# Kernel optimization log

Hardware: AMD Instinct MI355X
Metric: run time of the kernel (lower is better)

Reference implementation:

```python
import jax, jax.numpy as jnp
import numpy as np

D = 512            # token_dim * num_heads
TOKEN_DIM = 256
SCALE = TOKEN_DIM ** (-0.5)
EPS = 1e-12        # torch F.normalize eps
FIDX = (0, 1, 1)   # original bug: out_rv uses final_myo


def l2norm(x, axis):
    n = jnp.sqrt(jnp.sum(x * x, axis=axis, keepdims=True))
    return x / jnp.maximum(n, EPS)


def setup_inputs() -> dict:
    key = jax.random.key(0)
    ks = jax.random.split(key, 16)
    B, N = 16, 1024
    s = 0.02
    return {
        "x_lv": jax.random.normal(ks[0], (B, N, D), jnp.float32),
        "x_myo": jax.random.normal(ks[1], (B, N, D), jnp.float32),
        "x_rv": jax.random.normal(ks[2], (B, N, D), jnp.float32),
        # stacked per-branch params: branch 0=lv, 1=myo, 2=rv
        "Wq": jax.random.normal(ks[3], (3, D, D), jnp.float32) * s,
        "bq": jax.random.normal(ks[4], (3, D), jnp.float32) * s,
        "Wk": jax.random.normal(ks[5], (3, D, D), jnp.float32) * s,
        "bk": jax.random.normal(ks[6], (3, D), jnp.float32) * s,
        "wg": jax.random.normal(ks[7], (3, D, 1), jnp.float32),
        "Wp": jax.random.normal(ks[8], (3, 3, D, D), jnp.float32) * s,  # [branch, key_src]
        "bp": jax.random.normal(ks[9], (3, 3, D), jnp.float32) * s,
        "Wf": jax.random.normal(ks[10], (3, D, TOKEN_DIM), jnp.float32) * s,
        "bf": jax.random.normal(ks[11], (3, TOKEN_DIM), jnp.float32) * s,
    }


def reference(x_lv, x_myo, x_rv, Wq, bq, Wk, bk, wg, Wp, bp, Wf, bf):
    X = (x_lv, x_myo, x_rv)
    # projections + L2 normalize over feature dim
    Q = [l2norm(X[m] @ Wq[m] + bq[m], axis=-1) for m in range(3)]  # [B,N,D]
    K = [l2norm(X[m] @ Wk[m] + bk[m], axis=-1) for m in range(3)]  # [B,N,D]
    outs = []
    for m in range(3):
        A = l2norm((Q[m] @ wg[m]) * SCALE, axis=1)       # [B,N,1], normed over seq
        G = jnp.sum(A * Q[m], axis=1)[:, None, :]        # [B,1,D] (broadcast repeat)
        acc = Q[m]
        for j in range(3):
            acc = acc + (G * K[j]) @ Wp[m, j] + bp[m, j]
        outs.append(acc @ Wf[FIDX[m]] + bf[FIDX[m]])     # [B,N,token_dim]
    return tuple(outs)
```

## Files before the change

kernel.cpp:

```cpp
#include <hip/hip_runtime.h>
#include <hip/hip_bf16.h>

typedef __hip_bfloat16 bf16;
typedef __attribute__((ext_vector_type(8))) short short8;
typedef __attribute__((ext_vector_type(4))) float f32x4;

#define SCALE_F 0.0625f

__device__ __forceinline__ float b2f(short s) {
  union { float f; unsigned int u; } x;
  x.u = ((unsigned int)(unsigned short)s) << 16;
  return x.f;
}
__device__ __forceinline__ unsigned short f2bu(float f) {
  __hip_bfloat16 h = __float2bfloat16(f);
  unsigned short u;
  __builtin_memcpy(&u, &h, 2);
  return u;
}
__device__ __forceinline__ void store_out(float* p, float v) { *p = v; }
__device__ __forceinline__ void store_out(bf16* p, float v) { *p = __float2bfloat16(v); }

typedef __attribute__((address_space(3))) void lds_void;
typedef __attribute__((address_space(1))) void gbl_void;

__device__ __forceinline__ void lds_load16(void* l, const void* g) {
  __builtin_amdgcn_global_load_lds((const gbl_void*)g, (lds_void*)l, 16, 0, 0);
}

__device__ __forceinline__ void gemm256_xf32(
    const float* __restrict__ Af, int ldA,
    const bf16* __restrict__ Bt, int ldB,
    bf16* C, int ldC, const float* bias, int row0, int col0)
{
  __shared__ bf16 Abuf0[256 * 64], Abuf1[256 * 64];
  __shared__ bf16 Bbuf0[256 * 64], Bbuf1[256 * 64];
  const int tid = threadIdx.x;
  const int lane = tid & 63, w = tid >> 6;
  const int wm = w >> 2, wn = w & 3;
  const int lr = lane & 15, hi = lane >> 4;

  const int stageR = tid >> 3;
  const int cNat   = (tid & 7) << 3;
  const int cSwz   = ((tid & 7) ^ (stageR & 7)) << 3;
  const float* Ag0 = Af + (size_t)(row0 + stageR) * ldA + cNat;
  const bf16*  Bg0 = Bt + (size_t)(col0 + stageR) * ldB + cSwz;
  const int AwOff = stageR * 64 + cSwz;

  float4 prefE[8], prefO[8];
  auto issueA = [&](float4 (&dst)[8], int k0) {
#pragma unroll
    for (int q = 0; q < 4; ++q) {
      const float* p = Ag0 + (size_t)(q * 64) * ldA + k0;
      dst[q * 2 + 0] = *(const float4*)(p);
      dst[q * 2 + 1] = *(const float4*)(p + 4);
    }
  };
  auto writeA = [&](const float4 (&src)[8], bf16* Al) {
#pragma unroll
    for (int q = 0; q < 4; ++q) {
      float4 v0 = src[q * 2 + 0], v1 = src[q * 2 + 1];
      short8 o;
      o[0] = (short)f2bu(v0.x); o[1] = (short)f2bu(v0.y);
      o[2] = (short)f2bu(v0.z); o[3] = (short)f2bu(v0.w);
      o[4] = (short)f2bu(v1.x); o[5] = (short)f2bu(v1.y);
      o[6] = (short)f2bu(v1.z); o[7] = (short)f2bu(v1.w);
      *(short8*)&Al[AwOff + q * 4096] = o;
    }
  };
  auto stageB = [&](int bsel, int k0) {
    bf16* Bl = (bsel ? Bbuf1 : Bbuf0) + tid * 8;
    const bf16* Bg = Bg0 + k0;
#pragma unroll
    for (int q = 0; q < 4; ++q)
      lds_load16(Bl + q * 4096, Bg + (size_t)(q * 64) * ldB);
  };

  const int aoffb = (wm * 128 + lr) * 128;
  const int boffb = (wn * 64 + lr) * 128;
  const int s0 = ((hi ^ (lr & 7)) << 4);
  const int s1 = (((4 + hi) ^ (lr & 7)) << 4);

  f32x4 acc[8][4];
#pragma unroll
  for (int i = 0; i < 8; ++i)
#pragma unroll
    for (int j = 0; j < 4; ++j) acc[i][j] = (f32x4){0.f, 0.f, 0.f, 0.f};

  issueA(prefE, 0);
  issueA(prefO, 64);
  stageB(0, 0);
  stageB(1, 64);
  writeA(prefE, Abuf0);
  issueA(prefE, 128);
  writeA(prefO, Abuf1);
  asm volatile("s_waitcnt vmcnt(12)" ::: "memory");
  asm volatile("s_waitcnt lgkmcnt(0)" ::: "memory");
  __builtin_amdgcn_s_barrier();

#pragma unroll
  for (int t = 0; t < 8; ++t) {
    if (t + 3 < 8) {
      if (((t + 3) & 1) == 0) issueA(prefE, (t + 3) * 64);
      else                    issueA(prefO, (t + 3) * 64);
    }
    const char* Ab = (const char*)((t & 1) ? Abuf1 : Abuf0);
    const char* Bb = (const char*)((t & 1) ? Bbuf1 : Bbuf0);
    short8 ra[8], rb[4], ra2[8], rb2[4];
#pragma unroll
    for (int fr = 0; fr < 8; ++fr) ra[fr] = *(const short8*)(Ab + aoffb + fr * 2048 + s0);
#pragma unroll
    for (int fq = 0; fq < 4; ++fq) rb[fq] = *(const short8*)(Bb + boffb + fq * 2048 + s0);
    __builtin_amdgcn_s_setprio(1);
#pragma unroll
    for (int fr = 0; fr < 8; ++fr)
#pragma unroll
      for (int fq = 0; fq < 4; ++fq)
        acc[fr][fq] = __builtin_amdgcn_mfma_f32_16x16x32_bf16(ra[fr], rb[fq], acc[fr][fq], 0, 0, 0);
    __builtin_amdgcn_s_setprio(0);
#pragma unroll
    for (int fr = 0; fr < 8; ++fr) ra2[fr] = *(const short8*)(Ab + aoffb + fr * 2048 + s1);
#pragma unroll
    for (int fq = 0; fq < 4; ++fq) rb2[fq] = *(const short8*)(Bb + boffb + fq * 2048 + s1);
    asm volatile("s_waitcnt lgkmcnt(0)" ::: "memory");
    __builtin_amdgcn_s_barrier();
    if (t + 2 < 8) {
      if ((t & 1) == 0) writeA(prefE, Abuf0);
      else              writeA(prefO, Abuf1);
      stageB(t & 1, (t + 2) * 64);
    }
    __builtin_amdgcn_s_setprio(1);
#pragma unroll
    for (int fr = 0; fr < 8; ++fr)
#pragma unroll
      for (int fq = 0; fq < 4; ++fq)
        acc[fr][fq] = __builtin_amdgcn_mfma_f32_16x16x32_bf16(ra2[fr], rb2[fq], acc[fr][fq], 0, 0, 0);
    __builtin_amdgcn_s_setprio(0);
    if (t + 1 < 8) {
      if (t + 3 < 8)      asm volatile("s_waitcnt vmcnt(12)" ::: "memory");
      else if (t + 2 < 8) asm volatile("s_waitcnt vmcnt(4)"  ::: "memory");
      else                asm volatile("s_waitcnt vmcnt(0)"  ::: "memory");
      __builtin_amdgcn_s_barrier();
    }
  }

#pragma unroll
  for (int fr = 0; fr < 8; ++fr) {
    const int rowb = row0 + wm * 128 + fr * 16 + hi * 4;
#pragma unroll
    for (int fq = 0; fq < 4; ++fq) {
      const int col = col0 + wn * 64 + fq * 16 + lr;
      const float bv = bias[col];
      f32x4 v = acc[fr][fq];
#pragma unroll
      for (int r = 0; r < 4; ++r)
        store_out(&C[(size_t)(rowb + r) * ldC + col], v[r] + bv);
    }
  }
}

template<typename OutT>
__device__ __forceinline__ void gemm128p(
    const bf16* A0, const bf16* A1, const bf16* A2, const bf16* A3, int ldA,
    const bf16* Bt, int ldB, OutT* C, int ldC, const float* bias,
    int K, int row0, int col0)
{
  __shared__ bf16 Abuf0[128 * 64], Abuf1[128 * 64];
  __shared__ bf16 Bbuf0[128 * 64], Bbuf1[128 * 64];
  const int tid = threadIdx.x;
  const int lane = tid & 63, w = tid >> 6;
  const int wm = w >> 1, wn = w & 1;
  const int lr = lane & 15, hi = lane >> 4;

  const int stageR = tid >> 3;
  const int stageC = ((tid & 7) ^ (stageR & 7)) << 3;
  const bf16* Bg0 = Bt + (size_t)(col0 + stageR) * ldB + stageC;

  auto stage = [&](int bsel, int k0) {
    const int seg = k0 >> 9;
    const bf16* Aseg = (seg == 0) ? A0 : (seg == 1) ? A1 : (seg == 2) ? A2 : A3;
    const bf16* Ag = Aseg + (size_t)(row0 + stageR) * ldA + (k0 & 511) + stageC;
    const bf16* Bg = Bg0 + k0;
    bf16* Al = (bsel ? Abuf1 : Abuf0) + tid * 8;
    bf16* Bl = (bsel ? Bbuf1 : Bbuf0) + tid * 8;
#pragma unroll
    for (int q = 0; q < 4; ++q) {
      lds_load16(Al + q * 2048, Ag + (size_t)(q * 32) * ldA);
      lds_load16(Bl + q * 2048, Bg + (size_t)(q * 32) * ldB);
    }
  };

  const int aoffb = (wm * 64 + lr) * 128;
  const int boffb = (wn * 64 + lr) * 128;
  const int s0 = ((hi ^ (lr & 7)) << 4);
  const int s1 = (((4 + hi) ^ (lr & 7)) << 4);

  f32x4 acc[4][4];
#pragma unroll
  for (int i = 0; i < 4; ++i)
#pragma unroll
    for (int j = 0; j < 4; ++j) acc[i][j] = (f32x4){0.f, 0.f, 0.f, 0.f};

  const int nt = K >> 6;
  stage(0, 0);
  stage(1, 64);
  asm volatile("s_waitcnt vmcnt(8)" ::: "memory");
  __builtin_amdgcn_s_barrier();

  for (int t = 0; t < nt; ++t) {
    const char* Ab = (const char*)((t & 1) ? Abuf1 : Abuf0);
    const char* Bb = (const char*)((t & 1) ? Bbuf1 : Bbuf0);
    short8 ra[4], rb[4], ra2[4], rb2[4];
#pragma unroll
    for (int fr = 0; fr < 4; ++fr) ra[fr] = *(const short8*)(Ab + aoffb + fr * 2048 + s0);
#pragma unroll
    for (int fq = 0; fq < 4; ++fq) rb[fq] = *(const short8*)(Bb + boffb + fq * 2048 + s0);
    __builtin_amdgcn_s_setprio(1);
#pragma unroll
    for (int fr = 0; fr < 4; ++fr)
#pragma unroll
      for (int fq = 0; fq < 4; ++fq)
        acc[fr][fq] = __builtin_amdgcn_mfma_f32_16x16x32_bf16(ra[fr], rb[fq], acc[fr][fq], 0, 0, 0);
    __builtin_amdgcn_s_setprio(0);
#pragma unroll
    for (int fr = 0; fr < 4; ++fr) ra2[fr] = *(const short8*)(Ab + aoffb + fr * 2048 + s1);
#pragma unroll
    for (int fq = 0; fq < 4; ++fq) rb2[fq] = *(const short8*)(Bb + boffb + fq * 2048 + s1);
    asm volatile("s_waitcnt lgkmcnt(0)" ::: "memory");
    __builtin_amdgcn_s_barrier();
    if (t + 2 < nt) stage(t & 1, (t + 2) << 6);
    __builtin_amdgcn_s_setprio(1);
#pragma unroll
    for (int fr = 0; fr < 4; ++fr)
#pragma unroll
      for (int fq = 0; fq < 4; ++fq)
        acc[fr][fq] = __builtin_amdgcn_mfma_f32_16x16x32_bf16(ra2[fr], rb2[fq], acc[fr][fq], 0, 0, 0);
    __builtin_amdgcn_s_setprio(0);
    if (t + 1 < nt) {
      if (t + 2 < nt) asm volatile("s_waitcnt vmcnt(8)" ::: "memory");
      else            asm volatile("s_waitcnt vmcnt(0)" ::: "memory");
      __builtin_amdgcn_s_barrier();
    }
  }

#pragma unroll
  for (int fr = 0; fr < 4; ++fr) {
    const int rowb = row0 + wm * 64 + fr * 16 + hi * 4;
#pragma unroll
    for (int fq = 0; fq < 4; ++fq) {
      const int col = col0 + wn * 64 + fq * 16 + lr;
      const float bv = bias ? bias[col] : 0.f;
      f32x4 v = acc[fr][fq];
#pragma unroll
      for (int r = 0; r < 4; ++r)
        store_out(&C[(size_t)(rowb + r) * ldC + col], v[r] + bv);
    }
  }
}

template<typename OutT>
__device__ __forceinline__ void gemm_tile(
    const bf16* A0, int ldA, const bf16* Bt, int ldB, OutT* C, int ldC,
    const float* bias, int K, int row0, int col0)
{
  __shared__ bf16 As[128 * 32];
  __shared__ bf16 Bs[128 * 32];
  const int t = threadIdx.x;
  const int lane = t & 63;
  const int w = t >> 6;
  const int wm = w >> 1, wn = w & 1;
  const int lr = lane & 15, hi = lane >> 4;
  const int rA = t >> 2;
  const int kA = (t & 3) * 8;

  f32x4 acc[4][4];
#pragma unroll
  for (int i = 0; i < 4; ++i)
#pragma unroll
    for (int j = 0; j < 4; ++j) acc[i][j] = (f32x4){0.f, 0.f, 0.f, 0.f};

  const int nk = K >> 5;
  for (int kt = 0; kt < nk; ++kt) {
    const int k0 = kt << 5;
    __syncthreads();
    lds_load16(&As[t * 8],        A0 + (size_t)(row0 + rA) * ldA + k0 + kA);
    lds_load16(&As[2048 + t * 8], A0 + (size_t)(row0 + 64 + rA) * ldA + k0 + kA);
    lds_load16(&Bs[t * 8],        Bt + (size_t)(col0 + rA) * ldB + k0 + kA);
    lds_load16(&Bs[2048 + t * 8], Bt + (size_t)(col0 + 64 + rA) * ldB + k0 + kA);
    __syncthreads();
    short8 af[4], bfr[4];
#pragma unroll
    for (int f = 0; f < 4; ++f)
      af[f] = *(const short8*)&As[(wm * 64 + f * 16 + lr) * 32 + hi * 8];
#pragma unroll
    for (int f = 0; f < 4; ++f)
      bfr[f] = *(const short8*)&Bs[(wn * 64 + f * 16 + lr) * 32 + hi * 8];
#pragma unroll
    for (int i = 0; i < 4; ++i)
#pragma unroll
      for (int j = 0; j < 4; ++j)
        acc[i][j] = __builtin_amdgcn_mfma_f32_16x16x32_bf16(af[i], bfr[j], acc[i][j], 0, 0, 0);
  }

#pragma unroll
  for (int i = 0; i < 4; ++i) {
    const int rowb = row0 + wm * 64 + i * 16 + hi * 4;
#pragma unroll
    for (int j = 0; j < 4; ++j) {
      const int col = col0 + wn * 64 + j * 16 + lr;
      const float bv = bias ? bias[col] : 0.f;
      f32x4 v = acc[i][j];
#pragma unroll
      for (int r = 0; r < 4; ++r)
        store_out(&C[(size_t)(rowb + r) * ldC + col], v[r] + bv);
    }
  }
}

__global__ __launch_bounds__(256) void k_transpose(
    const float* __restrict__ in, bf16* __restrict__ out, int R, int C)
{
  const int tilesC = C >> 6;
  const int tr = (blockIdx.x / tilesC) << 6;
  const int tc = (blockIdx.x % tilesC) << 6;
  const size_t base = (size_t)blockIdx.y * R * C;
  __shared__ unsigned short tile[64][72];
  const int rr = threadIdx.x >> 4;
  const int cc = (threadIdx.x & 15) << 2;
#pragma unroll
  for (int p = 0; p < 4; ++p) {
    const int r = rr + (p << 4);
    float4 v = *(const float4*)&in[base + (size_t)(tr + r) * C + tc + cc];
    tile[cc + 0][r] = f2bu(v.x);
    tile[cc + 1][r] = f2bu(v.y);
    tile[cc + 2][r] = f2bu(v.z);
    tile[cc + 3][r] = f2bu(v.w);
  }
  __syncthreads();
#pragma unroll
  for (int p = 0; p < 4; ++p) {
    const int r = rr + (p << 4);
    ushort4 o;
    o.x = tile[r][cc + 0];
    o.y = tile[r][cc + 1];
    o.z = tile[r][cc + 2];
    o.w = tile[r][cc + 3];
    *(ushort4*)&out[base + (size_t)(tc + r) * R + tr + cc] = o;
  }
}

__global__ __launch_bounds__(256) void k_copy_bf16(
    const float* __restrict__ in, bf16* __restrict__ out)
{
  const long long i = (long long)blockIdx.x * 256 + threadIdx.x;
  float4 v = ((const float4*)in)[i];
  ushort4 o;
  o.x = f2bu(v.x); o.y = f2bu(v.y); o.z = f2bu(v.z); o.w = f2bu(v.w);
  ((ushort4*)out)[i] = o;
}

__global__ __launch_bounds__(256) void k_bprime(
    const float* __restrict__ bp, const float* __restrict__ Wf,
    const float* __restrict__ bfv, float* __restrict__ bpr)
{
  const int m = blockIdx.x;
  const int dc = blockIdx.y;
  const int n = threadIdx.x;
  const int fi = (m == 0) ? 0 : 1;
  float s = (dc == 0) ? bfv[fi * 256 + n] : 0.f;
  for (int d = dc * 64; d < dc * 64 + 64; ++d) {
    float b3 = bp[(m * 3 + 0) * 512 + d] + bp[(m * 3 + 1) * 512 + d] +
               bp[(m * 3 + 2) * 512 + d];
    s += b3 * Wf[(size_t)fi * 512 * 256 + (size_t)d * 256 + n];
  }
  atomicAdd(&bpr[m * 256 + n], s);
}

__global__ __launch_bounds__(512, 2) void k_gemm1(
    const float* __restrict__ x0, const float* __restrict__ x1,
    const float* __restrict__ x2, const bf16* __restrict__ WT,
    const float* __restrict__ bq, const float* __restrict__ bk,
    bf16* __restrict__ QK)
{
  const int bid = blockIdx.x;
  const int swz = (bid & 7) * 96 + (bid >> 3);
  const int m = swz >> 8;
  const int rem = swz & 255;
  const int tm = rem >> 2;
  const int tn = (rem >> 1) & 1;
  const int qk = rem & 1;
  const int inst = qk ? (m + 3) : m;
  const float* A = (m == 0) ? x0 : (m == 1) ? x1 : x2;
  const bf16* B = WT + (size_t)inst * (512 * 512);
  const float* bias = (qk ? bk : bq) + m * 512;
  bf16* C = QK + (size_t)inst * (16384 * 512);
  gemm256_xf32(A, 512, B, 512, C, 512, bias, tm * 256, tn * 256);
}

__global__ __launch_bounds__(256) void k_gemm_wpf(
    const bf16* __restrict__ WfT, const bf16* __restrict__ Wpbf,
    float* __restrict__ WpfT)
{
  const int inst = blockIdx.y;
  const int m = inst / 3;
  const int fi = (m == 0) ? 0 : 1;
  const int tm = blockIdx.x >> 2, tn = blockIdx.x & 3;
  const bf16* A = WfT + (size_t)fi * (256 * 512);
  const bf16* B = Wpbf + (size_t)inst * (512 * 512);
  float* C = WpfT + (size_t)inst * (256 * 512);
  gemm_tile<float>(A, 512, B, 512, C, 512, nullptr, 512, tm * 128, tn * 128);
}

__global__ __launch_bounds__(256, 2) void k_gemm2(
    const bf16* __restrict__ QK, const bf16* __restrict__ W2T,
    const float* __restrict__ bpr, float* __restrict__ out)
{
  const int bid = blockIdx.x;
  const int swz = (bid & 7) * 96 + (bid >> 3);
  const int e = swz >> 4;
  const int tm = (swz >> 1) & 7;
  const int tn = swz & 1;
  const int m = e / 16, b = e & 15;
  const bf16* A0 = QK + ((size_t)m * 16384 + (size_t)b * 1024) * 512;
  const bf16* A1 = QK + ((size_t)(3 * 16384) + (size_t)b * 1024) * 512;
  const bf16* A2 = QK + ((size_t)(4 * 16384) + (size_t)b * 1024) * 512;
  const bf16* A3 = QK + ((size_t)(5 * 16384) + (size_t)b * 1024) * 512;
  const bf16* Bt = W2T + (size_t)e * (256 * 2048);
  float* C = out + (size_t)e * (1024 * 256);
  gemm128p<float>(A0, A1, A2, A3, 512, Bt, 2048, C, 256, bpr + m * 256, 2048,
                  tm * 128, tn * 128);
}

__global__ __launch_bounds__(256) void k_norm(
    bf16* __restrict__ QK, const float* __restrict__ wg, float* __restrict__ qdot)
{
  const int row = blockIdx.x * 4 + (threadIdx.x >> 6);
  const int lane = threadIdx.x & 63;
  bf16* p = QK + (size_t)row * 512 + lane * 8;
  short8 v = *(const short8*)p;
  float f[8];
  float ss = 0.f;
#pragma unroll
  for (int i = 0; i < 8; ++i) { f[i] = b2f(v[i]); ss += f[i] * f[i]; }
#pragma unroll
  for (int o = 32; o; o >>= 1) ss += __shfl_xor(ss, o);
  const float inv = 1.f / fmaxf(sqrtf(ss), 1e-12f);
  short8 ov;
#pragma unroll
  for (int i = 0; i < 8; ++i) ov[i] = (short)f2bu(f[i] * inv);
  *(short8*)p = ov;
  const int tt = row >> 14;
  if (tt < 3) {
    const float* wgm = wg + (size_t)tt * 512 + lane * 8;
    float dot = 0.f;
#pragma unroll
    for (int i = 0; i < 8; ++i) dot += f[i] * wgm[i];
    dot *= inv;
#pragma unroll
    for (int o = 32; o; o >>= 1) dot += __shfl_xor(dot, o);
    if (lane == 0) qdot[row] = dot;
  }
}

__global__ __launch_bounds__(256) void k_G(
    const float* __restrict__ qdot, const bf16* __restrict__ QK, float* __restrict__ G)
{
  const int e = blockIdx.x;
  const int m = e >> 4, b = e & 15;
  const int d0 = blockIdx.y << 6;
  __shared__ float Al[1024];
  __shared__ float red[4];
  __shared__ float Gp[4][64];
  const int t = threadIdx.x;
  const float* qd = qdot + (size_t)m * 16384 + (size_t)b * 1024;
  float ss = 0.f;
#pragma unroll
  for (int i = 0; i < 4; ++i) {
    float x = qd[t + i * 256] * SCALE_F;
    Al[t + i * 256] = x;
    ss += x * x;
  }
#pragma unroll
  for (int o = 32; o; o >>= 1) ss += __shfl_xor(ss, o);
  if ((t & 63) == 0) red[t >> 6] = ss;
  __syncthreads();
  const float inv = 1.f / fmaxf(sqrtf(red[0] + red[1] + red[2] + red[3]), 1e-12f);

  const int d = d0 + (t & 63);
  const int q = t >> 6;
  const bf16* Qb = QK + ((size_t)m * 16384 + (size_t)b * 1024) * 512 + d;
  float g = 0.f;
  for (int n = q * 256; n < q * 256 + 256; ++n)
    g += Al[n] * b2f(*(const short*)&Qb[(size_t)n * 512]);
  Gp[q][t & 63] = g;
  __syncthreads();
  if (t < 64)
    G[(size_t)e * 512 + d0 + t] = (Gp[0][t] + Gp[1][t] + Gp[2][t] + Gp[3][t]) * inv;
}

__global__ __launch_bounds__(256) void k_w2t(
    const bf16* __restrict__ WfT, const float* __restrict__ WpfT,
    const float* __restrict__ G, bf16* __restrict__ W2T)
{
  const int e = blockIdx.x;
  const int m = e >> 4;
  const int fi = (m == 0) ? 0 : 1;
  const int t = threadIdx.x;
  bf16* out = W2T + (size_t)e * (256 * 2048);
  __shared__ float Gl[512];
  Gl[t] = G[(size_t)e * 512 + t];
  Gl[t + 256] = G[(size_t)e * 512 + t + 256];
  __syncthreads();
  const int k = t * 8;
  for (int nr = 0; nr < 16; ++nr) {
    const int n = blockIdx.y * 16 + nr;
    if (k < 512) {
      *(short8*)&out[(size_t)n * 2048 + k] =
          *(const short8*)&WfT[((size_t)fi * 256 + n) * 512 + k];
    } else {
      const int j = (k >> 9) - 1;
      const int d = k & 511;
      const float* src = WpfT + (((size_t)(m * 3 + j) * 256 + n) * 512 + d);
      short8 o;
#pragma unroll
      for (int i = 0; i < 8; ++i) o[i] = (short)f2bu(Gl[d + i] * src[i]);
      *(short8*)&out[(size_t)n * 2048 + k] = o;
    }
  }
}

extern "C" void kernel_launch(void* const* d_in, const int* in_sizes, int n_in,
                              void* d_out, int out_size, void* d_ws, size_t ws_size,
                              hipStream_t stream) {
  const float* x_lv = (const float*)d_in[0];
  const float* x_myo = (const float*)d_in[1];
  const float* x_rv = (const float*)d_in[2];
  const float* Wq = (const float*)d_in[3];
  const float* bq = (const float*)d_in[4];
  const float* Wk = (const float*)d_in[5];
  const float* bk = (const float*)d_in[6];
  const float* wg = (const float*)d_in[7];
  const float* Wp = (const float*)d_in[8];
  const float* bp = (const float*)d_in[9];
  const float* Wf = (const float*)d_in[10];
  const float* bfv = (const float*)d_in[11];
  float* out = (float*)d_out;

  char* ws = (char*)d_ws;
  bf16* QK    = (bf16*)(ws);
  bf16* W2T   = (bf16*)(ws + 100663296);
  bf16* WT    = (bf16*)(ws + 150994944);
  bf16* Wpbf  = (bf16*)(ws + 154140672);
  bf16* WfT   = (bf16*)(ws + 158859264);
  float* WpfT = (float*)(ws + 159383552);
  float* qdot = (float*)(ws + 164102144);
  float* G    = (float*)(ws + 164298752);
  float* bpr  = (float*)(ws + 164397056);

  k_transpose<<<dim3(64, 3), 256, 0, stream>>>(Wq, WT, 512, 512);
  k_transpose<<<dim3(64, 3), 256, 0, stream>>>(Wk, WT + 3 * 512 * 512, 512, 512);
  k_transpose<<<dim3(32, 2), 256, 0, stream>>>(Wf, WfT, 512, 256);
  k_copy_bf16<<<2304, 256, 0, stream>>>(Wp, Wpbf);
  hipMemsetAsync(bpr, 0, 3 * 256 * sizeof(float), stream);
  k_bprime<<<dim3(3, 8), 256, 0, stream>>>(bp, Wf, bfv, bpr);

  k_gemm1<<<768, 512, 0, stream>>>(x_lv, x_myo, x_rv, WT, bq, bk, QK);

  k_norm<<<24576, 256, 0, stream>>>(QK, wg, qdot);

  k_gemm_wpf<<<dim3(8, 9), 256, 0, stream>>>(WfT, Wpbf, WpfT);

  k_G<<<dim3(48, 8), 256, 0, stream>>>(qdot, QK, G);

  k_w2t<<<dim3(48, 16), 256, 0, stream>>>(WfT, WpfT, G, W2T);

  k_gemm2<<<768, 256, 0, stream>>>(QK, W2T, bpr, out);
}
```

Baseline: 388.8 us.

## Pre-convert inputs to bf16 in fused prep kernel and use async LDS loads in gemm1

Merges the weight transposes, Wp conversion, bias precomputation and a new fp32-to-bf16 conversion of the three activation inputs into one prep kernel. The first GEMM then reads bf16 activations through direct global-to-LDS loads instead of converting fp32 in registers. The bias atomics and memset are replaced by per-chunk partial sums that the second GEMM adds at its epilogue. This removes several launches and the register conversion path, but adds a full extra read and write pass over the activations. The W2T buffer now reuses the Xbf workspace region.

```diff
diff --git a/kernel.cpp b/kernel.cpp
--- a/kernel.cpp
+++ b/kernel.cpp
@@ -28,148 +28,17 @@
   __builtin_amdgcn_global_load_lds((const gbl_void*)g, (lds_void*)l, 16, 0, 0);
 }
 
-__device__ __forceinline__ void gemm256_xf32(
-    const float* __restrict__ Af, int ldA,
-    const bf16* __restrict__ Bt, int ldB,
-    bf16* C, int ldC, const float* bias, int row0, int col0)
+template<typename OutT>
+__device__ __forceinline__ void gemm256_tile(
+    const bf16* A0, const bf16* A1, const bf16* A2, const bf16* A3, int ldA,
+    const bf16* Bt, int ldB, OutT* C, int ldC, const float* bias,
+    int K, int row0, int col0)
 {
   __shared__ bf16 Abuf0[256 * 64], Abuf1[256 * 64];
   __shared__ bf16 Bbuf0[256 * 64], Bbuf1[256 * 64];
   const int tid = threadIdx.x;
   const int lane = tid & 63, w = tid >> 6;
   const int wm = w >> 2, wn = w & 3;
-  const int lr = lane & 15, hi = lane >> 4;
-
-  const int stageR = tid >> 3;
-  const int cNat   = (tid & 7) << 3;
-  const int cSwz   = ((tid & 7) ^ (stageR & 7)) << 3;
-  const float* Ag0 = Af + (size_t)(row0 + stageR) * ldA + cNat;
-  const bf16*  Bg0 = Bt + (size_t)(col0 + stageR) * ldB + cSwz;
-  const int AwOff = stageR * 64 + cSwz;
-
-  float4 prefE[8], prefO[8];
-  auto issueA = [&](float4 (&dst)[8], int k0) {
-#pragma unroll
-    for (int q = 0; q < 4; ++q) {
-      const float* p = Ag0 + (size_t)(q * 64) * ldA + k0;
-      dst[q * 2 + 0] = *(const float4*)(p);
-      dst[q * 2 + 1] = *(const float4*)(p + 4);
-    }
-  };
-  auto writeA = [&](const float4 (&src)[8], bf16* Al) {
-#pragma unroll
-    for (int q = 0; q < 4; ++q) {
-      float4 v0 = src[q * 2 + 0], v1 = src[q * 2 + 1];
-      short8 o;
-      o[0] = (short)f2bu(v0.x); o[1] = (short)f2bu(v0.y);
-      o[2] = (short)f2bu(v0.z); o[3] = (short)f2bu(v0.w);
-      o[4] = (short)f2bu(v1.x); o[5] = (short)f2bu(v1.y);
-      o[6] = (short)f2bu(v1.z); o[7] = (short)f2bu(v1.w);
-      *(short8*)&Al[AwOff + q * 4096] = o;
-    }
-  };
-  auto stageB = [&](int bsel, int k0) {
-    bf16* Bl = (bsel ? Bbuf1 : Bbuf0) + tid * 8;
-    const bf16* Bg = Bg0 + k0;
-#pragma unroll
-    for (int q = 0; q < 4; ++q)
-      lds_load16(Bl + q * 4096, Bg + (size_t)(q * 64) * ldB);
-  };
-
-  const int aoffb = (wm * 128 + lr) * 128;
-  const int boffb = (wn * 64 + lr) * 128;
-  const int s0 = ((hi ^ (lr & 7)) << 4);
-  const int s1 = (((4 + hi) ^ (lr & 7)) << 4);
-
-  f32x4 acc[8][4];
-#pragma unroll
-  for (int i = 0; i < 8; ++i)
-#pragma unroll
-    for (int j = 0; j < 4; ++j) acc[i][j] = (f32x4){0.f, 0.f, 0.f, 0.f};
-
-  issueA(prefE, 0);
-  issueA(prefO, 64);
-  stageB(0, 0);
-  stageB(1, 64);
-  writeA(prefE, Abuf0);
-  issueA(prefE, 128);
-  writeA(prefO, Abuf1);
-  asm volatile("s_waitcnt vmcnt(12)" ::: "memory");
-  asm volatile("s_waitcnt lgkmcnt(0)" ::: "memory");
-  __builtin_amdgcn_s_barrier();
-
-#pragma unroll
-  for (int t = 0; t < 8; ++t) {
-    if (t + 3 < 8) {
-      if (((t + 3) & 1) == 0) issueA(prefE, (t + 3) * 64);
-      else                    issueA(prefO, (t + 3) * 64);
-    }
-    const char* Ab = (const char*)((t & 1) ? Abuf1 : Abuf0);
-    const char* Bb = (const char*)((t & 1) ? Bbuf1 : Bbuf0);
-    short8 ra[8], rb[4], ra2[8], rb2[4];
-#pragma unroll
-    for (int fr = 0; fr < 8; ++fr) ra[fr] = *(const short8*)(Ab + aoffb + fr * 2048 + s0);
-#pragma unroll
-    for (int fq = 0; fq < 4; ++fq) rb[fq] = *(const short8*)(Bb + boffb + fq * 2048 + s0);
-    __builtin_amdgcn_s_setprio(1);
-#pragma unroll
-    for (int fr = 0; fr < 8; ++fr)
-#pragma unroll
-      for (int fq = 0; fq < 4; ++fq)
-        acc[fr][fq] = __builtin_amdgcn_mfma_f32_16x16x32_bf16(ra[fr], rb[fq], acc[fr][fq], 0, 0, 0);
-    __builtin_amdgcn_s_setprio(0);
-#pragma unroll
-    for (int fr = 0; fr < 8; ++fr) ra2[fr] = *(const short8*)(Ab + aoffb + fr * 2048 + s1);
-#pragma unroll
-    for (int fq = 0; fq < 4; ++fq) rb2[fq] = *(const short8*)(Bb + boffb + fq * 2048 + s1);
-    asm volatile("s_waitcnt lgkmcnt(0)" ::: "memory");
-    __builtin_amdgcn_s_barrier();
-    if (t + 2 < 8) {
-      if ((t & 1) == 0) writeA(prefE, Abuf0);
-      else              writeA(prefO, Abuf1);
-      stageB(t & 1, (t + 2) * 64);
-    }
-    __builtin_amdgcn_s_setprio(1);
-#pragma unroll
-    for (int fr = 0; fr < 8; ++fr)
-#pragma unroll
-      for (int fq = 0; fq < 4; ++fq)
-        acc[fr][fq] = __builtin_amdgcn_mfma_f32_16x16x32_bf16(ra2[fr], rb2[fq], acc[fr][fq], 0, 0, 0);
-    __builtin_amdgcn_s_setprio(0);
-    if (t + 1 < 8) {
-      if (t + 3 < 8)      asm volatile("s_waitcnt vmcnt(12)" ::: "memory");
-      else if (t + 2 < 8) asm volatile("s_waitcnt vmcnt(4)"  ::: "memory");
-      else                asm volatile("s_waitcnt vmcnt(0)"  ::: "memory");
-      __builtin_amdgcn_s_barrier();
-    }
-  }
-
-#pragma unroll
-  for (int fr = 0; fr < 8; ++fr) {
-    const int rowb = row0 + wm * 128 + fr * 16 + hi * 4;
-#pragma unroll
-    for (int fq = 0; fq < 4; ++fq) {
-      const int col = col0 + wn * 64 + fq * 16 + lr;
-      const float bv = bias[col];
-      f32x4 v = acc[fr][fq];
-#pragma unroll
-      for (int r = 0; r < 4; ++r)
-        store_out(&C[(size_t)(rowb + r) * ldC + col], v[r] + bv);
-    }
-  }
-}
-
-template<typename OutT>
-__device__ __forceinline__ void gemm128p(
-    const bf16* A0, const bf16* A1, const bf16* A2, const bf16* A3, int ldA,
-    const bf16* Bt, int ldB, OutT* C, int ldC, const float* bias,
-    int K, int row0, int col0)
-{
-  __shared__ bf16 Abuf0[128 * 64], Abuf1[128 * 64];
-  __shared__ bf16 Bbuf0[128 * 64], Bbuf1[128 * 64];
-  const int tid = threadIdx.x;
-  const int lane = tid & 63, w = tid >> 6;
-  const int wm = w >> 1, wn = w & 1;
   const int lr = lane & 15, hi = lane >> 4;
 
   const int stageR = tid >> 3;
@@ -185,19 +54,19 @@
     bf16* Bl = (bsel ? Bbuf1 : Bbuf0) + tid * 8;
 #pragma unroll
     for (int q = 0; q < 4; ++q) {
-      lds_load16(Al + q * 2048, Ag + (size_t)(q * 32) * ldA);
-      lds_load16(Bl + q * 2048, Bg + (size_t)(q * 32) * ldB);
+      lds_load16(Al + q * 4096, Ag + (size_t)q * 64 * ldA);
+      lds_load16(Bl + q * 4096, Bg + (size_t)q * 64 * ldB);
     }
   };
 
-  const int aoffb = (wm * 64 + lr) * 128;
+  const int aoffb = (wm * 128 + lr) * 128;
   const int boffb = (wn * 64 + lr) * 128;
   const int s0 = ((hi ^ (lr & 7)) << 4);
   const int s1 = (((4 + hi) ^ (lr & 7)) << 4);
 
-  f32x4 acc[4][4];
-#pragma unroll
-  for (int i = 0; i < 4; ++i)
+  f32x4 acc[8][4];
+#pragma unroll
+  for (int i = 0; i < 8; ++i)
 #pragma unroll
     for (int j = 0; j < 4; ++j) acc[i][j] = (f32x4){0.f, 0.f, 0.f, 0.f};
 
@@ -210,20 +79,20 @@
   for (int t = 0; t < nt; ++t) {
     const char* Ab = (const char*)((t & 1) ? Abuf1 : Abuf0);
     const char* Bb = (const char*)((t & 1) ? Bbuf1 : Bbuf0);
-    short8 ra[4], rb[4], ra2[4], rb2[4];
-#pragma unroll
-    for (int fr = 0; fr < 4; ++fr) ra[fr] = *(const short8*)(Ab + aoffb + fr * 2048 + s0);
+    short8 ra[8], rb[4], ra2[8], rb2[4];
+#pragma unroll
+    for (int fr = 0; fr < 8; ++fr) ra[fr] = *(const short8*)(Ab + aoffb + fr * 2048 + s0);
 #pragma unroll
     for (int fq = 0; fq < 4; ++fq) rb[fq] = *(const short8*)(Bb + boffb + fq * 2048 + s0);
     __builtin_amdgcn_s_setprio(1);
 #pragma unroll
-    for (int fr = 0; fr < 4; ++fr)
+    for (int fr = 0; fr < 8; ++fr)
 #pragma unroll
       for (int fq = 0; fq < 4; ++fq)
         acc[fr][fq] = __builtin_amdgcn_mfma_f32_16x16x32_bf16(ra[fr], rb[fq], acc[fr][fq], 0, 0, 0);
     __builtin_amdgcn_s_setprio(0);
 #pragma unroll
-    for (int fr = 0; fr < 4; ++fr) ra2[fr] = *(const short8*)(Ab + aoffb + fr * 2048 + s1);
+    for (int fr = 0; fr < 8; ++fr) ra2[fr] = *(const short8*)(Ab + aoffb + fr * 2048 + s1);
 #pragma unroll
     for (int fq = 0; fq < 4; ++fq) rb2[fq] = *(const short8*)(Bb + boffb + fq * 2048 + s1);
     asm volatile("s_waitcnt lgkmcnt(0)" ::: "memory");
@@ -231,7 +100,7 @@
     if (t + 2 < nt) stage(t & 1, (t + 2) << 6);
     __builtin_amdgcn_s_setprio(1);
 #pragma unroll
-    for (int fr = 0; fr < 4; ++fr)
+    for (int fr = 0; fr < 8; ++fr)
 #pragma unroll
       for (int fq = 0; fq < 4; ++fq)
         acc[fr][fq] = __builtin_amdgcn_mfma_f32_16x16x32_bf16(ra2[fr], rb2[fq], acc[fr][fq], 0, 0, 0);
@@ -244,12 +113,115 @@
   }
 
 #pragma unroll
-  for (int fr = 0; fr < 4; ++fr) {
-    const int rowb = row0 + wm * 64 + fr * 16 + hi * 4;
+  for (int fr = 0; fr < 8; ++fr) {
+    const int rowb = row0 + wm * 128 + fr * 16 + hi * 4;
 #pragma unroll
     for (int fq = 0; fq < 4; ++fq) {
       const int col = col0 + wn * 64 + fq * 16 + lr;
       const float bv = bias ? bias[col] : 0.f;
+      f32x4 v = acc[fr][fq];
+#pragma unroll
+      for (int r = 0; r < 4; ++r)
+        store_out(&C[(size_t)(rowb + r) * ldC + col], v[r] + bv);
+    }
+  }
+}
+
+template<typename OutT, int BREP>
+__device__ __forceinline__ void gemm128p(
+    const bf16* A0, const bf16* A1, const bf16* A2, const bf16* A3, int ldA,
+    const bf16* Bt, int ldB, OutT* C, int ldC, const float* bias,
+    int K, int row0, int col0)
+{
+  __shared__ bf16 Abuf0[128 * 64], Abuf1[128 * 64];
+  __shared__ bf16 Bbuf0[128 * 64], Bbuf1[128 * 64];
+  const int tid = threadIdx.x;
+  const int lane = tid & 63, w = tid >> 6;
+  const int wm = w >> 1, wn = w & 1;
+  const int lr = lane & 15, hi = lane >> 4;
+
+  const int stageR = tid >> 3;
+  const int stageC = ((tid & 7) ^ (stageR & 7)) << 3;
+  const bf16* Bg0 = Bt + (size_t)(col0 + stageR) * ldB + stageC;
+
+  auto stage = [&](int bsel, int k0) {
+    const int seg = k0 >> 9;
+    const bf16* Aseg = (seg == 0) ? A0 : (seg == 1) ? A1 : (seg == 2) ? A2 : A3;
+    const bf16* Ag = Aseg + (size_t)(row0 + stageR) * ldA + (k0 & 511) + stageC;
+    const bf16* Bg = Bg0 + k0;
+    bf16* Al = (bsel ? Abuf1 : Abuf0) + tid * 8;
+    bf16* Bl = (bsel ? Bbuf1 : Bbuf0) + tid * 8;
+#pragma unroll
+    for (int q = 0; q < 4; ++q) {
+      lds_load16(Al + q * 2048, Ag + (size_t)(q * 32) * ldA);
+      lds_load16(Bl + q * 2048, Bg + (size_t)(q * 32) * ldB);
+    }
+  };
+
+  const int aoffb = (wm * 64 + lr) * 128;
+  const int boffb = (wn * 64 + lr) * 128;
+  const int s0 = ((hi ^ (lr & 7)) << 4);
+  const int s1 = (((4 + hi) ^ (lr & 7)) << 4);
+
+  f32x4 acc[4][4];
+#pragma unroll
+  for (int i = 0; i < 4; ++i)
+#pragma unroll
+    for (int j = 0; j < 4; ++j) acc[i][j] = (f32x4){0.f, 0.f, 0.f, 0.f};
+
+  const int nt = K >> 6;
+  stage(0, 0);
+  stage(1, 64);
+  asm volatile("s_waitcnt vmcnt(8)" ::: "memory");
+  __builtin_amdgcn_s_barrier();
+
+  for (int t = 0; t < nt; ++t) {
+    const char* Ab = (const char*)((t & 1) ? Abuf1 : Abuf0);
+    const char* Bb = (const char*)((t & 1) ? Bbuf1 : Bbuf0);
+    short8 ra[4], rb[4], ra2[4], rb2[4];
+#pragma unroll
+    for (int fr = 0; fr < 4; ++fr) ra[fr] = *(const short8*)(Ab + aoffb + fr * 2048 + s0);
+#pragma unroll
+    for (int fq = 0; fq < 4; ++fq) rb[fq] = *(const short8*)(Bb + boffb + fq * 2048 + s0);
+    __builtin_amdgcn_s_setprio(1);
+#pragma unroll
+    for (int fr = 0; fr < 4; ++fr)
+#pragma unroll
+      for (int fq = 0; fq < 4; ++fq)
+        acc[fr][fq] = __builtin_amdgcn_mfma_f32_16x16x32_bf16(ra[fr], rb[fq], acc[fr][fq], 0, 0, 0);
+    __builtin_amdgcn_s_setprio(0);
+#pragma unroll
+    for (int fr = 0; fr < 4; ++fr) ra2[fr] = *(const short8*)(Ab + aoffb + fr * 2048 + s1);
+#pragma unroll
+    for (int fq = 0; fq < 4; ++fq) rb2[fq] = *(const short8*)(Bb + boffb + fq * 2048 + s1);
+    asm volatile("s_waitcnt lgkmcnt(0)" ::: "memory");
+    __builtin_amdgcn_s_barrier();
+    if (t + 2 < nt) stage(t & 1, (t + 2) << 6);
+    __builtin_amdgcn_s_setprio(1);
+#pragma unroll
+    for (int fr = 0; fr < 4; ++fr)
+#pragma unroll
+      for (int fq = 0; fq < 4; ++fq)
+        acc[fr][fq] = __builtin_amdgcn_mfma_f32_16x16x32_bf16(ra2[fr], rb2[fq], acc[fr][fq], 0, 0, 0);
+    __builtin_amdgcn_s_setprio(0);
+    if (t + 1 < nt) {
+      if (t + 2 < nt) asm volatile("s_waitcnt vmcnt(8)" ::: "memory");
+      else            asm volatile("s_waitcnt vmcnt(0)" ::: "memory");
+      __builtin_amdgcn_s_barrier();
+    }
+  }
+
+#pragma unroll
+  for (int fr = 0; fr < 4; ++fr) {
+    const int rowb = row0 + wm * 64 + fr * 16 + hi * 4;
+#pragma unroll
+    for (int fq = 0; fq < 4; ++fq) {
+      const int col = col0 + wn * 64 + fq * 16 + lr;
+      float bv = 0.f;
+      if (bias) {
+#pragma unroll
+        for (int i = 0; i < BREP; ++i) bv += bias[i * 256 + col];
+      }
       f32x4 v = acc[fr][fq];
 #pragma unroll
       for (int r = 0; r < 4; ++r)
@@ -317,68 +289,90 @@
   }
 }
 
-__global__ __launch_bounds__(256) void k_transpose(
-    const float* __restrict__ in, bf16* __restrict__ out, int R, int C)
-{
-  const int tilesC = C >> 6;
-  const int tr = (blockIdx.x / tilesC) << 6;
-  const int tc = (blockIdx.x % tilesC) << 6;
-  const size_t base = (size_t)blockIdx.y * R * C;
+__global__ __launch_bounds__(256) void k_prep(
+    const float* __restrict__ x0, const float* __restrict__ x1,
+    const float* __restrict__ x2, bf16* __restrict__ xbf,
+    const float* __restrict__ Wq, const float* __restrict__ Wk,
+    const float* __restrict__ Wf, const float* __restrict__ Wp,
+    const float* __restrict__ bp, const float* __restrict__ bfv,
+    bf16* __restrict__ WT, bf16* __restrict__ WfT,
+    bf16* __restrict__ Wpbf, float* __restrict__ bprp)
+{
   __shared__ unsigned short tile[64][72];
-  const int rr = threadIdx.x >> 4;
-  const int cc = (threadIdx.x & 15) << 2;
-#pragma unroll
-  for (int p = 0; p < 4; ++p) {
-    const int r = rr + (p << 4);
-    float4 v = *(const float4*)&in[base + (size_t)(tr + r) * C + tc + cc];
-    tile[cc + 0][r] = f2bu(v.x);
-    tile[cc + 1][r] = f2bu(v.y);
-    tile[cc + 2][r] = f2bu(v.z);
-    tile[cc + 3][r] = f2bu(v.w);
-  }
-  __syncthreads();
-#pragma unroll
-  for (int p = 0; p < 4; ++p) {
-    const int r = rr + (p << 4);
+  const int bid = blockIdx.x;
+  const int t = threadIdx.x;
+
+  if (bid >= 1048) {
+    const long long i = (long long)(bid - 1048) * 256 + t;
+    const int tt = (int)(i / 2097152);
+    const long long e = i - (long long)tt * 2097152;
+    const float4* src = (const float4*)(tt == 0 ? x0 : tt == 1 ? x1 : x2);
+    float4 v = src[e];
     ushort4 o;
-    o.x = tile[r][cc + 0];
-    o.y = tile[r][cc + 1];
-    o.z = tile[r][cc + 2];
-    o.w = tile[r][cc + 3];
-    *(ushort4*)&out[base + (size_t)(tc + r) * R + tr + cc] = o;
-  }
-}
-
-__global__ __launch_bounds__(256) void k_copy_bf16(
-    const float* __restrict__ in, bf16* __restrict__ out)
-{
-  const long long i = (long long)blockIdx.x * 256 + threadIdx.x;
-  float4 v = ((const float4*)in)[i];
-  ushort4 o;
-  o.x = f2bu(v.x); o.y = f2bu(v.y); o.z = f2bu(v.z); o.w = f2bu(v.w);
-  ((ushort4*)out)[i] = o;
-}
-
-__global__ __launch_bounds__(256) void k_bprime(
-    const float* __restrict__ bp, const float* __restrict__ Wf,
-    const float* __restrict__ bfv, float* __restrict__ bpr)
-{
-  const int m = blockIdx.x;
-  const int dc = blockIdx.y;
-  const int n = threadIdx.x;
-  const int fi = (m == 0) ? 0 : 1;
-  float s = (dc == 0) ? bfv[fi * 256 + n] : 0.f;
-  for (int d = dc * 64; d < dc * 64 + 64; ++d) {
-    float b3 = bp[(m * 3 + 0) * 512 + d] + bp[(m * 3 + 1) * 512 + d] +
-               bp[(m * 3 + 2) * 512 + d];
-    s += b3 * Wf[(size_t)fi * 512 * 256 + (size_t)d * 256 + n];
-  }
-  atomicAdd(&bpr[m * 256 + n], s);
+    o.x = f2bu(v.x); o.y = f2bu(v.y); o.z = f2bu(v.z); o.w = f2bu(v.w);
+    ((ushort4*)xbf)[i] = o;
+    return;
+  }
+  if (bid < 448) {
+    const float* in; bf16* out; int R, C, ti;
+    if (bid < 192)      { in = Wq + (bid / 64) * 262144; out = WT + (bid / 64) * 262144; R = 512; C = 512; ti = bid & 63; }
+    else if (bid < 384) { int b2 = bid - 192; in = Wk + (b2 / 64) * 262144; out = WT + (3 + b2 / 64) * 262144; R = 512; C = 512; ti = b2 & 63; }
+    else                { int b2 = bid - 384; in = Wf + (b2 / 32) * 131072; out = WfT + (b2 / 32) * 131072; R = 512; C = 256; ti = b2 & 31; }
+    const int tilesC = C >> 6;
+    const int tr = (ti / tilesC) << 6;
+    const int tc = (ti % tilesC) << 6;
+    const int rr = t >> 4;
+    const int cc = (t & 15) << 2;
+#pragma unroll
+    for (int p = 0; p < 4; ++p) {
+      const int r = rr + (p << 4);
+      float4 v = *(const float4*)&in[(size_t)(tr + r) * C + tc + cc];
+      tile[cc + 0][r] = f2bu(v.x);
+      tile[cc + 1][r] = f2bu(v.y);
+      tile[cc + 2][r] = f2bu(v.z);
+      tile[cc + 3][r] = f2bu(v.w);
+    }
+    __syncthreads();
+#pragma unroll
+    for (int p = 0; p < 4; ++p) {
+      const int r = rr + (p << 4);
+      ushort4 o;
+      o.x = tile[r][cc + 0];
+      o.y = tile[r][cc + 1];
+      o.z = tile[r][cc + 2];
+      o.w = tile[r][cc + 3];
+      *(ushort4*)&out[(size_t)(tc + r) * R + tr + cc] = o;
+    }
+    return;
+  }
+  if (bid < 1024) {
+    const int base = (bid - 448) * 256 + t;
+#pragma unroll
+    for (int s = 0; s < 4; ++s) {
+      const int i = base + s * 147456;
+      float4 v = ((const float4*)Wp)[i];
+      ushort4 o;
+      o.x = f2bu(v.x); o.y = f2bu(v.y); o.z = f2bu(v.z); o.w = f2bu(v.w);
+      ((ushort4*)Wpbf)[i] = o;
+    }
+    return;
+  }
+  {
+    const int mm = (bid - 1024) >> 3, dc = (bid - 1024) & 7;
+    const int n = t;
+    const int fi = (mm == 0) ? 0 : 1;
+    float s = (dc == 0) ? bfv[fi * 256 + n] : 0.f;
+    for (int d = dc * 64; d < dc * 64 + 64; ++d) {
+      float b3 = bp[(mm * 3 + 0) * 512 + d] + bp[(mm * 3 + 1) * 512 + d] +
+                 bp[(mm * 3 + 2) * 512 + d];
+      s += b3 * Wf[(size_t)fi * 512 * 256 + (size_t)d * 256 + n];
+    }
+    bprp[(mm * 8 + dc) * 256 + n] = s;
+  }
 }
 
 __global__ __launch_bounds__(512, 2) void k_gemm1(
-    const float* __restrict__ x0, const float* __restrict__ x1,
-    const float* __restrict__ x2, const bf16* __restrict__ WT,
+    const bf16* __restrict__ Xbf, const bf16* __restrict__ WT,
     const float* __restrict__ bq, const float* __restrict__ bk,
     bf16* __restrict__ QK)
 {
@@ -390,11 +384,11 @@
   const int tn = (rem >> 1) & 1;
   const int qk = rem & 1;
   const int inst = qk ? (m + 3) : m;
-  const float* A = (m == 0) ? x0 : (m == 1) ? x1 : x2;
+  const bf16* A = Xbf + (size_t)m * (16384 * 512);
   const bf16* B = WT + (size_t)inst * (512 * 512);
   const float* bias = (qk ? bk : bq) + m * 512;
   bf16* C = QK + (size_t)inst * (16384 * 512);
-  gemm256_xf32(A, 512, B, 512, C, 512, bias, tm * 256, tn * 256);
+  gemm256_tile<bf16>(A, A, A, A, 512, B, 512, C, 512, bias, 512, tm * 256, tn * 256);
 }
 
 __global__ __launch_bounds__(256) void k_gemm_wpf(
@@ -413,7 +407,7 @@
 
 __global__ __launch_bounds__(256, 2) void k_gemm2(
     const bf16* __restrict__ QK, const bf16* __restrict__ W2T,
-    const float* __restrict__ bpr, float* __restrict__ out)
+    const float* __restrict__ bprp, float* __restrict__ out)
 {
   const int bid = blockIdx.x;
   const int swz = (bid & 7) * 96 + (bid >> 3);
@@ -427,8 +421,8 @@
   const bf16* A3 = QK + ((size_t)(5 * 16384) + (size_t)b * 1024) * 512;
   const bf16* Bt = W2T + (size_t)e * (256 * 2048);
   float* C = out + (size_t)e * (1024 * 256);
-  gemm128p<float>(A0, A1, A2, A3, 512, Bt, 2048, C, 256, bpr + m * 256, 2048,
-                  tm * 128, tn * 128);
+  gemm128p<float, 8>(A0, A1, A2, A3, 512, Bt, 2048, C, 256, bprp + m * 2048, 2048,
+                     tm * 128, tn * 128);
 }
 
 __global__ __launch_bounds__(256) void k_norm(
@@ -548,23 +542,20 @@
 
   char* ws = (char*)d_ws;
   bf16* QK    = (bf16*)(ws);
-  bf16* W2T   = (bf16*)(ws + 100663296);
+  bf16* Xbf   = (bf16*)(ws + 100663296);
   bf16* WT    = (bf16*)(ws + 150994944);
   bf16* Wpbf  = (bf16*)(ws + 154140672);
   bf16* WfT   = (bf16*)(ws + 158859264);
   float* WpfT = (float*)(ws + 159383552);
   float* qdot = (float*)(ws + 164102144);
   float* G    = (float*)(ws + 164298752);
-  float* bpr  = (float*)(ws + 164397056);
-
-  k_transpose<<<dim3(64, 3), 256, 0, stream>>>(Wq, WT, 512, 512);
-  k_transpose<<<dim3(64, 3), 256, 0, stream>>>(Wk, WT + 3 * 512 * 512, 512, 512);
-  k_transpose<<<dim3(32, 2), 256, 0, stream>>>(Wf, WfT, 512, 256);
-  k_copy_bf16<<<2304, 256, 0, stream>>>(Wp, Wpbf);
-  hipMemsetAsync(bpr, 0, 3 * 256 * sizeof(float), stream);
-  k_bprime<<<dim3(3, 8), 256, 0, stream>>>(bp, Wf, bfv, bpr);
-
-  k_gemm1<<<768, 512, 0, stream>>>(x_lv, x_myo, x_rv, WT, bq, bk, QK);
+  float* bprp = (float*)(ws + 164397056);
+  bf16* W2T   = Xbf;
+
+  k_prep<<<25624, 256, 0, stream>>>(x_lv, x_myo, x_rv, Xbf, Wq, Wk, Wf, Wp,
+                                    bp, bfv, WT, WfT, Wpbf, bprp);
+
+  k_gemm1<<<768, 512, 0, stream>>>(Xbf, WT, bq, bk, QK);
 
   k_norm<<<24576, 256, 0, stream>>>(QK, wg, qdot);
 
@@ -574,5 +565,5 @@
 
   k_w2t<<<dim3(48, 16), 256, 0, stream>>>(WfT, WpfT, G, W2T);
 
-  k_gemm2<<<768, 256, 0, stream>>>(QK, W2T, bpr, out);
-}
+  k_gemm2<<<768, 256, 0, stream>>>(QK, W2T, bprp, out);
+}
```

Result: faster. 366.4 us (-5.8%).
